# Optimization experiments

Hardware: AMD Instinct MI355X
Metric: run time of the kernel (lower is better)

## Reference

```python
import jax, jax.numpy as jnp
import numpy as np

B, L, D, N = 32, 512, 512, 8  # batch, length, input_size, num_labels


def setup_inputs() -> dict:
    key = jax.random.key(0)
    k1, k2, k3, k4, k5 = jax.random.split(key, 5)
    scale = 0.02
    return {
        "input_h": jax.random.normal(k1, (B, L, D), dtype=jnp.float32),
        "input_c": jax.random.normal(k2, (B, L, D), dtype=jnp.float32),
        "mask": jnp.ones((B, L), dtype=jnp.float32),
        "U": jax.random.normal(k3, (N, D, D), dtype=jnp.float32) * scale,
        "W_d": jax.random.normal(k4, (N, D), dtype=jnp.float32) * scale,
        "W_e": jax.random.normal(k5, (N, D), dtype=jnp.float32) * scale,
        "b": jnp.zeros((N, 1, 1), dtype=jnp.float32),
    }


def reference(input_h, input_c, mask, U, W_d, W_e, b):
    # Biaffine attention (NeuroNLP2 BiAAttention): head = decoder side, child = encoder side.
    # bilinear term: [b, n, l_head, l_child]
    out = jnp.einsum("bld,nde,bme->bnlm", input_h, U, input_c)
    # linear head term -> broadcast over child axis
    out = out + jnp.einsum("nd,bld->bnl", W_d, input_h)[:, :, :, None]
    # linear child term -> broadcast over head axis
    out = out + jnp.einsum("nd,bmd->bnm", W_e, input_c)[:, :, None, :]
    out = out + b[None]  # bias [n,1,1]
    # mask_d / mask_e multiplicative masking
    out = out * mask[:, None, :, None] * mask[:, None, None, :]
    # -inf on the diagonal (no self-arcs)
    length = out.shape[-1]
    diag = jnp.where(jnp.eye(length, dtype=bool), -jnp.inf, 0.0).astype(out.dtype)
    return out + diag
```

## Files before the change

kernel.cpp:

```cpp
#include <hip/hip_runtime.h>


#define B_ 32
#define L_ 512
#define D_ 512
#define N_ 8
#define MT 64
#define STR 536

using f16x8 = __attribute__((ext_vector_type(8))) _Float16;
using f32x4 = __attribute__((ext_vector_type(4))) float;
using u16x8 = __attribute__((ext_vector_type(8))) unsigned short;

static __device__ __forceinline__ float bf2f(unsigned short h) {
  union { unsigned u; float f; } v; v.u = (unsigned)h << 16; return v.f;
}
static __device__ __forceinline__ float h2f(unsigned short h) {
  _Float16 x; __builtin_memcpy(&x, &h, 2); return (float)x;
}
static __device__ __forceinline__ unsigned short f2h(float f) {
  _Float16 x = (_Float16)f; unsigned short u; __builtin_memcpy(&u, &x, 2); return u;
}

static __device__ __forceinline__ int sniff(const unsigned* mkw) {
  const unsigned w = *mkw;
  if (w == 0x3F800000u) return 0;
  if (w == 0x3C003C00u) return 1;
  if (w == 0x3F803F80u) return 2;
  return 1;
}

static __device__ __forceinline__ float ldscal(const void* base, int idx, int flag) {
  if (flag == 0) return ((const float*)base)[idx];
  const unsigned short u = ((const unsigned short*)base)[idx];
  return (flag == 1) ? h2f(u) : bf2f(u);
}

__global__ __launch_bounds__(256)
void cvt_f16(const void* __restrict__ src, unsigned short* __restrict__ dst, int n8,
             const unsigned* __restrict__ mkw) {
  const int flag = sniff(mkw);
  int i = blockIdx.x * 256 + threadIdx.x;
  const int stride = gridDim.x * 256;
  for (; i < n8; i += stride) {
    u16x8 o;
    if (flag == 1) {
      o = ((const u16x8*)src)[i];
    } else if (flag == 0) {
      const float4* s = (const float4*)src + 2 * (size_t)i;
      float4 a = s[0], b = s[1];
      o[0]=f2h(a.x); o[1]=f2h(a.y); o[2]=f2h(a.z); o[3]=f2h(a.w);
      o[4]=f2h(b.x); o[5]=f2h(b.y); o[6]=f2h(b.z); o[7]=f2h(b.w);
    } else {
      u16x8 v = ((const u16x8*)src)[i];
#pragma unroll
      for (int j = 0; j < 8; ++j) o[j] = f2h(bf2f(v[j]));
    }
    *(u16x8*)(dst + 8 * (size_t)i) = o;
  }
}

template <bool CVT>
__global__ __launch_bounds__(512)
void biaffine(const unsigned short* __restrict__ Hc, const void* __restrict__ Hr,
              const unsigned short* __restrict__ Cc, const void* __restrict__ Cr,
              const unsigned short* __restrict__ Uc, const void* __restrict__ Ur,
              const void* __restrict__ Mk, const void* __restrict__ Wd,
              const void* __restrict__ We, const void* __restrict__ Bia,
              unsigned short* __restrict__ Out)
{
  __shared__ __align__(16) unsigned short cpb[64 * STR];
  __shared__ float wev[512], wdv[512], mlv[512], psum[512];
  __shared__ float colterm[64], mcv[64];

  const int flag = sniff((const unsigned*)Mk);
  const int tid  = threadIdx.x;
  const int wave = tid >> 6;
  const int lane = tid & 63;
  const int quad = lane >> 4;
  const int l16  = lane & 15;

  const int bid = blockIdx.x;
  const int n  = bid & 7;
  const int mt = (bid >> 3) & 7;
  const int b  = bid >> 6;

  const size_t cOff = ((size_t)b * L_ + mt * MT) * D_;
  const size_t hOff = (size_t)b * L_ * D_;
  const size_t uOff = (size_t)n * D_ * D_;

  auto ld8 = [&](const void* base, size_t off) -> u16x8 {
    u16x8 o;
    if (flag == 1) {
      o = *(const u16x8*)((const unsigned short*)base + off);
    } else if (flag == 0) {
      const float4* p = (const float4*)((const float*)base + off);
      float4 a = p[0], bq = p[1];
      o[0]=f2h(a.x); o[1]=f2h(a.y); o[2]=f2h(a.z); o[3]=f2h(a.w);
      o[4]=f2h(bq.x); o[5]=f2h(bq.y); o[6]=f2h(bq.z); o[7]=f2h(bq.w);
    } else {
      u16x8 v = *(const u16x8*)((const unsigned short*)base + off);
#pragma unroll
      for (int j = 0; j < 8; ++j) o[j] = f2h(bf2f(v[j]));
    }
    return o;
  };

  {
    const int row = tid >> 3, cb0 = (tid & 7) * 64;
    u16x8* dst = (u16x8*)&cpb[row * STR + cb0];
#pragma unroll
    for (int j = 0; j < 8; ++j) {
      if constexpr (CVT) dst[j] = ld8(Cr, cOff + (size_t)row * D_ + cb0 + j * 8);
      else               dst[j] = ((const u16x8*)(Cc + cOff + (size_t)row * D_ + cb0))[j];
    }
  }
  wev[tid] = ldscal(We, n * D_ + tid, flag);
  wdv[tid] = ldscal(Wd, n * D_ + tid, flag);
  mlv[tid] = ldscal(Mk, b * L_ + tid, flag);
  if (tid < 64) mcv[tid] = ldscal(Mk, b * L_ + mt * MT + tid, flag);
  __syncthreads();

  {
    const int m = tid >> 3, e0 = (tid & 7) * 64;
    float s = 0.f;
#pragma unroll 8
    for (int e = 0; e < 64; ++e) s += h2f(cpb[m * STR + e0 + e]) * wev[e0 + e];
    psum[tid] = s;
  }
  __syncthreads();
  if (tid < 64) {
    float s = ldscal(Bia, n, flag);
#pragma unroll
    for (int j = 0; j < 8; ++j) s += psum[tid * 8 + j];
    colterm[tid] = s;
  }

  f32x4 acc[4][4];
#pragma unroll
  for (int i = 0; i < 4; ++i)
#pragma unroll
    for (int j = 0; j < 4; ++j) acc[i][j] = (f32x4){0.f, 0.f, 0.f, 0.f};

  {
    size_t uo[4];
#pragma unroll
    for (int di = 0; di < 4; ++di)
      uo[di] = uOff + (size_t)((4 * wave + di) * 16 + l16) * D_ + quad * 8;

    auto ldU = [&](int di, int s) -> f16x8 {
      if constexpr (CVT) { u16x8 t = ld8(Ur, uo[di] + (size_t)s * 32); return *(f16x8*)&t; }
      else               return *(const f16x8*)(Uc + uo[di] + (size_t)s * 32);
    };

    f16x8 bB[2][4];
#pragma unroll
    for (int di = 0; di < 4; ++di) bB[0][di] = ldU(di, 0);

#pragma unroll
    for (int s = 0; s < 16; ++s) {
      const int cur = s & 1;
      if (s < 15) {
#pragma unroll
        for (int di = 0; di < 4; ++di) bB[cur ^ 1][di] = ldU(di, s + 1);
      }
      f16x8 aF[4];
#pragma unroll
      for (int mi = 0; mi < 4; ++mi)
        aF[mi] = *(const f16x8*)&cpb[(mi * 16 + l16) * STR + s * 32 + quad * 8];
#pragma unroll
      for (int mi = 0; mi < 4; ++mi)
#pragma unroll
        for (int di = 0; di < 4; ++di)
          acc[mi][di] = __builtin_amdgcn_mfma_f32_16x16x32_f16(aF[mi], bB[cur][di], acc[mi][di], 0, 0, 0);
    }
  }
  __syncthreads();

#pragma unroll
  for (int di = 0; di < 4; ++di) {
    const int d_g = (4 * wave + di) * 16 + l16;
    const float wd = wdv[d_g];
#pragma unroll
    for (int mi = 0; mi < 4; ++mi)
#pragma unroll
      for (int r = 0; r < 4; ++r) {
        const int m_loc = mi * 16 + quad * 4 + r;
        cpb[m_loc * STR + d_g] = f2h(acc[mi][di][r] + wd);
      }
  }
  __syncthreads();

  f32x4 acc2[4][4];
#pragma unroll
  for (int i = 0; i < 4; ++i)
#pragma unroll
    for (int j = 0; j < 4; ++j) acc2[i][j] = (f32x4){0.f, 0.f, 0.f, 0.f};

  {
    size_t ho[4];
#pragma unroll
    for (int li = 0; li < 4; ++li)
      ho[li] = hOff + (size_t)((4 * wave + li) * 16 + l16) * D_ + quad * 8;

    auto ldH = [&](int li, int s) -> f16x8 {
      if constexpr (CVT) { u16x8 t = ld8(Hr, ho[li] + (size_t)s * 32); return *(f16x8*)&t; }
      else               return *(const f16x8*)(Hc + ho[li] + (size_t)s * 32);
    };

    f16x8 aB[2][4];
#pragma unroll
    for (int li = 0; li < 4; ++li) aB[0][li] = ldH(li, 0);

#pragma unroll
    for (int s = 0; s < 16; ++s) {
      const int cur = s & 1;
      if (s < 15) {
#pragma unroll
        for (int li = 0; li < 4; ++li) aB[cur ^ 1][li] = ldH(li, s + 1);
      }
      f16x8 bF[4];
#pragma unroll
      for (int mj = 0; mj < 4; ++mj)
        bF[mj] = *(const f16x8*)&cpb[(mj * 16 + l16) * STR + s * 32 + quad * 8];
#pragma unroll
      for (int li = 0; li < 4; ++li)
#pragma unroll
        for (int mj = 0; mj < 4; ++mj)
          acc2[li][mj] = __builtin_amdgcn_mfma_f32_16x16x32_f16(aB[cur][li], bF[mj], acc2[li][mj], 0, 0, 0);
    }
  }

  const size_t outBase = (size_t)(b * N_ + n) * L_ * L_;
#pragma unroll
  for (int mj = 0; mj < 4; ++mj) {
    const int m_loc = mj * 16 + l16;
    const int m_g = mt * MT + m_loc;
    const float cm = colterm[m_loc];
    const float mm = mcv[m_loc];
#pragma unroll
    for (int li = 0; li < 4; ++li)
#pragma unroll
      for (int r = 0; r < 4; ++r) {
        const int l = (4 * wave + li) * 16 + quad * 4 + r;
        const float v = (acc2[li][mj][r] + cm) * (mlv[l] * mm);
        const unsigned short us = (l == m_g) ? (unsigned short)0xFBFFu : f2h(v);
        Out[outBase + (size_t)l * L_ + m_g] = us;
      }
  }
}

extern "C" void kernel_launch(void* const* d_in, const int* in_sizes, int n_in,
                              void* d_out, int out_size, void* d_ws, size_t ws_size,
                              hipStream_t stream) {
  const void* Hr  = d_in[0];
  const void* Cr  = d_in[1];
  const void* Mk  = d_in[2];
  const void* Ur  = d_in[3];
  const void* Wd  = d_in[4];
  const void* We  = d_in[5];
  const void* Bia = d_in[6];
  unsigned short* Out = (unsigned short*)d_out;
  (void)in_sizes; (void)n_in; (void)out_size;

  const size_t nH = (size_t)B_ * L_ * D_;
  const size_t nC = nH;
  const size_t nU = (size_t)N_ * D_ * D_;
  const size_t needBytes = (nH + nC + nU) * sizeof(unsigned short);

  dim3 grid(B_ * N_ * (L_ / MT));
  dim3 block(512);

  if (ws_size >= needBytes) {
    unsigned short* Hc = (unsigned short*)d_ws;
    unsigned short* Cc = Hc + nH;
    unsigned short* Uc = Cc + nC;
    const unsigned* mkw = (const unsigned*)Mk;
    cvt_f16<<<1024, 256, 0, stream>>>(Hr, Hc, (int)(nH / 8), mkw);
    cvt_f16<<<1024, 256, 0, stream>>>(Cr, Cc, (int)(nC / 8), mkw);
    cvt_f16<<<512,  256, 0, stream>>>(Ur, Uc, (int)(nU / 8), mkw);
    biaffine<false><<<grid, block, 0, stream>>>(Hc, nullptr, Cc, nullptr, Uc, nullptr,
                                                Mk, Wd, We, Bia, Out);
  } else {
    biaffine<true><<<grid, block, 0, stream>>>(nullptr, Hr, nullptr, Cr, nullptr, Ur,
                                               Mk, Wd, We, Bia, Out);
  }
}
```

Before: 575.6 us.

## Precompute child linear term in C conversion pass and merge conversion kernels

Adds a prep_c kernel that converts input_c to fp16 and computes the W_e·c + bias column term for all labels in one pass. The main biaffine kernel can then load that term instead of recomputing it per block with an extra sync. The H and U conversions are merged into one launch, the first U and H fragment loads are issued earlier, and s_setprio is placed around the MFMA bursts. The cost is an extra workspace buffer and a new code path that only runs when the workspace is large enough.

```diff
diff --git a/kernel.cpp b/kernel.cpp
--- a/kernel.cpp
+++ b/kernel.cpp
@@ -34,6 +34,23 @@
   if (flag == 0) return ((const float*)base)[idx];
   const unsigned short u = ((const unsigned short*)base)[idx];
   return (flag == 1) ? h2f(u) : bf2f(u);
+}
+
+static __device__ __forceinline__ u16x8 ld8f(const void* base, size_t off, int flag) {
+  u16x8 o;
+  if (flag == 1) {
+    o = *(const u16x8*)((const unsigned short*)base + off);
+  } else if (flag == 0) {
+    const float4* p = (const float4*)((const float*)base + off);
+    float4 a = p[0], bq = p[1];
+    o[0]=f2h(a.x); o[1]=f2h(a.y); o[2]=f2h(a.z); o[3]=f2h(a.w);
+    o[4]=f2h(bq.x); o[5]=f2h(bq.y); o[6]=f2h(bq.z); o[7]=f2h(bq.w);
+  } else {
+    u16x8 v = *(const u16x8*)((const unsigned short*)base + off);
+#pragma unroll
+    for (int j = 0; j < 8; ++j) o[j] = f2h(bf2f(v[j]));
+  }
+  return o;
 }
 
 __global__ __launch_bounds__(256)
@@ -43,34 +60,94 @@
   int i = blockIdx.x * 256 + threadIdx.x;
   const int stride = gridDim.x * 256;
   for (; i < n8; i += stride) {
-    u16x8 o;
-    if (flag == 1) {
-      o = ((const u16x8*)src)[i];
-    } else if (flag == 0) {
-      const float4* s = (const float4*)src + 2 * (size_t)i;
-      float4 a = s[0], b = s[1];
-      o[0]=f2h(a.x); o[1]=f2h(a.y); o[2]=f2h(a.z); o[3]=f2h(a.w);
-      o[4]=f2h(b.x); o[5]=f2h(b.y); o[6]=f2h(b.z); o[7]=f2h(b.w);
-    } else {
-      u16x8 v = ((const u16x8*)src)[i];
-#pragma unroll
-      for (int j = 0; j < 8; ++j) o[j] = f2h(bf2f(v[j]));
-    }
+    u16x8 o = ld8f(src, 8 * (size_t)i, flag);
     *(u16x8*)(dst + 8 * (size_t)i) = o;
   }
 }
 
-template <bool CVT>
+__global__ __launch_bounds__(256)
+void cvt_f16_2(const void* __restrict__ s0, unsigned short* __restrict__ d0, int n0,
+               const void* __restrict__ s1, unsigned short* __restrict__ d1, int n1,
+               const unsigned* __restrict__ mkw) {
+  const int flag = sniff(mkw);
+  int i = blockIdx.x * 256 + threadIdx.x;
+  const int stride = gridDim.x * 256;
+  const int tot = n0 + n1;
+  for (; i < tot; i += stride) {
+    const void* src; unsigned short* dst; int k;
+    if (i < n0) { src = s0; dst = d0; k = i; }
+    else        { src = s1; dst = d1; k = i - n0; }
+    u16x8 o = ld8f(src, 8 * (size_t)k, flag);
+    *(u16x8*)(dst + 8 * (size_t)k) = o;
+  }
+}
+
+__global__ __launch_bounds__(256)
+void prep_c(const void* __restrict__ Cr, unsigned short* __restrict__ Cc,
+            float* __restrict__ CTp, const void* __restrict__ We,
+            const void* __restrict__ Bia, const unsigned* __restrict__ mkw)
+{
+  __shared__ float wetab[N_ * 512];
+  __shared__ float psum[256 * 9];
+  const int flag = sniff(mkw);
+  const int tid = threadIdx.x;
+  const int b  = blockIdx.x >> 4;
+  const int mc = blockIdx.x & 15;
+
+  for (int i = tid; i < N_ * 512; i += 256) wetab[i] = ldscal(We, i, flag);
+  __syncthreads();
+
+  const int ml = tid >> 3;
+  const int e8 = tid & 7;
+  const int m  = mc * 32 + ml;
+  const size_t rowOff = ((size_t)b * L_ + m) * D_;
+
+  float pn[N_];
+#pragma unroll
+  for (int nn = 0; nn < N_; ++nn) pn[nn] = 0.f;
+
+#pragma unroll
+  for (int j = 0; j < 8; ++j) {
+    const int e0 = (j * 8 + e8) * 8;
+    u16x8 v = ld8f(Cr, rowOff + e0, flag);
+    *(u16x8*)(Cc + rowOff + e0) = v;
+    float cf[8];
+#pragma unroll
+    for (int k = 0; k < 8; ++k) cf[k] = h2f(v[k]);
+#pragma unroll
+    for (int nn = 0; nn < N_; ++nn) {
+      float s = pn[nn];
+#pragma unroll
+      for (int k = 0; k < 8; ++k) s += cf[k] * wetab[nn * 512 + e0 + k];
+      pn[nn] = s;
+    }
+  }
+#pragma unroll
+  for (int nn = 0; nn < N_; ++nn) psum[tid * 9 + nn] = pn[nn];
+  __syncthreads();
+
+  {
+    const int row = tid >> 3, nn = tid & 7;
+    float s = ldscal(Bia, nn, flag);
+#pragma unroll
+    for (int q = 0; q < 8; ++q) s += psum[(row * 8 + q) * 9 + nn];
+    CTp[((size_t)(b * N_ + nn)) * L_ + mc * 32 + row] = s;
+  }
+}
+
+template <bool CVT, bool CT>
 __global__ __launch_bounds__(512)
 void biaffine(const unsigned short* __restrict__ Hc, const void* __restrict__ Hr,
               const unsigned short* __restrict__ Cc, const void* __restrict__ Cr,
               const unsigned short* __restrict__ Uc, const void* __restrict__ Ur,
+              const float* __restrict__ CTp,
               const void* __restrict__ Mk, const void* __restrict__ Wd,
               const void* __restrict__ We, const void* __restrict__ Bia,
               unsigned short* __restrict__ Out)
 {
   __shared__ __align__(16) unsigned short cpb[64 * STR];
-  __shared__ float wev[512], wdv[512], mlv[512], psum[512];
+  __shared__ float wdv[512], mlv[512];
+  __shared__ float wev[512], psum[512];
   __shared__ float colterm[64], mcv[64];
 
   const int flag = sniff((const unsigned*)Mk);
@@ -89,51 +166,59 @@
   const size_t hOff = (size_t)b * L_ * D_;
   const size_t uOff = (size_t)n * D_ * D_;
 
-  auto ld8 = [&](const void* base, size_t off) -> u16x8 {
-    u16x8 o;
-    if (flag == 1) {
-      o = *(const u16x8*)((const unsigned short*)base + off);
-    } else if (flag == 0) {
-      const float4* p = (const float4*)((const float*)base + off);
-      float4 a = p[0], bq = p[1];
-      o[0]=f2h(a.x); o[1]=f2h(a.y); o[2]=f2h(a.z); o[3]=f2h(a.w);
-      o[4]=f2h(bq.x); o[5]=f2h(bq.y); o[6]=f2h(bq.z); o[7]=f2h(bq.w);
-    } else {
-      u16x8 v = *(const u16x8*)((const unsigned short*)base + off);
-#pragma unroll
-      for (int j = 0; j < 8; ++j) o[j] = f2h(bf2f(v[j]));
-    }
-    return o;
+  auto ld8 = [&](const void* base, size_t off) -> u16x8 { return ld8f(base, off, flag); };
+
+  size_t uo[4];
+#pragma unroll
+  for (int di = 0; di < 4; ++di)
+    uo[di] = uOff + (size_t)((4 * wave + di) * 16 + l16) * D_ + quad * 8;
+
+  auto ldU = [&](int di, int s) -> f16x8 {
+    if constexpr (CVT) { u16x8 t = ld8(Ur, uo[di] + (size_t)s * 32); return *(f16x8*)&t; }
+    else               return *(const f16x8*)(Uc + uo[di] + (size_t)s * 32);
   };
+
+  f16x8 bB[2][4];
+#pragma unroll
+  for (int di = 0; di < 4; ++di) bB[0][di] = ldU(di, 0);
 
   {
     const int row = tid >> 3, cb0 = (tid & 7) * 64;
+    u16x8 t[8];
+#pragma unroll
+    for (int j = 0; j < 8; ++j) {
+      if constexpr (CVT) t[j] = ld8(Cr, cOff + (size_t)row * D_ + cb0 + j * 8);
+      else               t[j] = ((const u16x8*)(Cc + cOff + (size_t)row * D_ + cb0))[j];
+    }
     u16x8* dst = (u16x8*)&cpb[row * STR + cb0];
 #pragma unroll
-    for (int j = 0; j < 8; ++j) {
-      if constexpr (CVT) dst[j] = ld8(Cr, cOff + (size_t)row * D_ + cb0 + j * 8);
-      else               dst[j] = ((const u16x8*)(Cc + cOff + (size_t)row * D_ + cb0))[j];
-    }
-  }
-  wev[tid] = ldscal(We, n * D_ + tid, flag);
+    for (int j = 0; j < 8; ++j) dst[j] = t[j];
+  }
   wdv[tid] = ldscal(Wd, n * D_ + tid, flag);
   mlv[tid] = ldscal(Mk, b * L_ + tid, flag);
   if (tid < 64) mcv[tid] = ldscal(Mk, b * L_ + mt * MT + tid, flag);
-  __syncthreads();
-
-  {
-    const int m = tid >> 3, e0 = (tid & 7) * 64;
-    float s = 0.f;
+  if constexpr (CT) {
+    if (tid < 64) colterm[tid] = CTp[((size_t)(b * N_ + n)) * L_ + mt * MT + tid];
+  } else {
+    wev[tid] = ldscal(We, n * D_ + tid, flag);
+  }
+  __syncthreads();
+
+  if constexpr (!CT) {
+    {
+      const int m = tid >> 3, e0 = (tid & 7) * 64;
+      float s = 0.f;
 #pragma unroll 8
-    for (int e = 0; e < 64; ++e) s += h2f(cpb[m * STR + e0 + e]) * wev[e0 + e];
-    psum[tid] = s;
-  }
-  __syncthreads();
-  if (tid < 64) {
-    float s = ldscal(Bia, n, flag);
-#pragma unroll
-    for (int j = 0; j < 8; ++j) s += psum[tid * 8 + j];
-    colterm[tid] = s;
+      for (int e = 0; e < 64; ++e) s += h2f(cpb[m * STR + e0 + e]) * wev[e0 + e];
+      psum[tid] = s;
+    }
+    __syncthreads();
+    if (tid < 64) {
+      float s = ldscal(Bia, n, flag);
+#pragma unroll
+      for (int j = 0; j < 8; ++j) s += psum[tid * 8 + j];
+      colterm[tid] = s;
+    }
   }
 
   f32x4 acc[4][4];
@@ -142,39 +227,40 @@
 #pragma unroll
     for (int j = 0; j < 4; ++j) acc[i][j] = (f32x4){0.f, 0.f, 0.f, 0.f};
 
-  {
-    size_t uo[4];
-#pragma unroll
-    for (int di = 0; di < 4; ++di)
-      uo[di] = uOff + (size_t)((4 * wave + di) * 16 + l16) * D_ + quad * 8;
-
-    auto ldU = [&](int di, int s) -> f16x8 {
-      if constexpr (CVT) { u16x8 t = ld8(Ur, uo[di] + (size_t)s * 32); return *(f16x8*)&t; }
-      else               return *(const f16x8*)(Uc + uo[di] + (size_t)s * 32);
-    };
-
-    f16x8 bB[2][4];
-#pragma unroll
-    for (int di = 0; di < 4; ++di) bB[0][di] = ldU(di, 0);
-
-#pragma unroll
-    for (int s = 0; s < 16; ++s) {
-      const int cur = s & 1;
-      if (s < 15) {
-#pragma unroll
-        for (int di = 0; di < 4; ++di) bB[cur ^ 1][di] = ldU(di, s + 1);
-      }
-      f16x8 aF[4];
-#pragma unroll
-      for (int mi = 0; mi < 4; ++mi)
-        aF[mi] = *(const f16x8*)&cpb[(mi * 16 + l16) * STR + s * 32 + quad * 8];
-#pragma unroll
-      for (int mi = 0; mi < 4; ++mi)
-#pragma unroll
-        for (int di = 0; di < 4; ++di)
-          acc[mi][di] = __builtin_amdgcn_mfma_f32_16x16x32_f16(aF[mi], bB[cur][di], acc[mi][di], 0, 0, 0);
-    }
-  }
+#pragma unroll
+  for (int s = 0; s < 16; ++s) {
+    const int cur = s & 1;
+    if (s < 15) {
+#pragma unroll
+      for (int di = 0; di < 4; ++di) bB[cur ^ 1][di] = ldU(di, s + 1);
+    }
+    f16x8 aF[4];
+#pragma unroll
+    for (int mi = 0; mi < 4; ++mi)
+      aF[mi] = *(const f16x8*)&cpb[(mi * 16 + l16) * STR + s * 32 + quad * 8];
+    __builtin_amdgcn_s_setprio(1);
+#pragma unroll
+    for (int mi = 0; mi < 4; ++mi)
+#pragma unroll
+      for (int di = 0; di < 4; ++di)
+        acc[mi][di] = __builtin_amdgcn_mfma_f32_16x16x32_f16(aF[mi], bB[cur][di], acc[mi][di], 0, 0, 0);
+    __builtin_amdgcn_s_setprio(0);
+  }
+
+  size_t ho[4];
+#pragma unroll
+  for (int li = 0; li < 4; ++li)
+    ho[li] = hOff + (size_t)((4 * wave + li) * 16 + l16) * D_ + quad * 8;
+
+  auto ldH = [&](int li, int s) -> f16x8 {
+    if constexpr (CVT) { u16x8 t = ld8(Hr, ho[li] + (size_t)s * 32); return *(f16x8*)&t; }
+    else               return *(const f16x8*)(Hc + ho[li] + (size_t)s * 32);
+  };
+
+  f16x8 aB[2][4];
+#pragma unroll
+  for (int li = 0; li < 4; ++li) aB[0][li] = ldH(li, 0);
+
   __syncthreads();
 
 #pragma unroll
@@ -197,38 +283,24 @@
 #pragma unroll
     for (int j = 0; j < 4; ++j) acc2[i][j] = (f32x4){0.f, 0.f, 0.f, 0.f};
 
-  {
-    size_t ho[4];
+#pragma unroll
+  for (int s = 0; s < 16; ++s) {
+    const int cur = s & 1;
+    if (s < 15) {
+#pragma unroll
+      for (int li = 0; li < 4; ++li) aB[cur ^ 1][li] = ldH(li, s + 1);
+    }
+    f16x8 bF[4];
+#pragma unroll
+    for (int mj = 0; mj < 4; ++mj)
+      bF[mj] = *(const f16x8*)&cpb[(mj * 16 + l16) * STR + s * 32 + quad * 8];
+    __builtin_amdgcn_s_setprio(1);
 #pragma unroll
     for (int li = 0; li < 4; ++li)
-      ho[li] = hOff + (size_t)((4 * wave + li) * 16 + l16) * D_ + quad * 8;
-
-    auto ldH = [&](int li, int s) -> f16x8 {
-      if constexpr (CVT) { u16x8 t = ld8(Hr, ho[li] + (size_t)s * 32); return *(f16x8*)&t; }
-      else               return *(const f16x8*)(Hc + ho[li] + (size_t)s * 32);
-    };
-
-    f16x8 aB[2][4];
-#pragma unroll
-    for (int li = 0; li < 4; ++li) aB[0][li] = ldH(li, 0);
-
-#pragma unroll
-    for (int s = 0; s < 16; ++s) {
-      const int cur = s & 1;
-      if (s < 15) {
-#pragma unroll
-        for (int li = 0; li < 4; ++li) aB[cur ^ 1][li] = ldH(li, s + 1);
-      }
-      f16x8 bF[4];
 #pragma unroll
       for (int mj = 0; mj < 4; ++mj)
-        bF[mj] = *(const f16x8*)&cpb[(mj * 16 + l16) * STR + s * 32 + quad * 8];
-#pragma unroll
-      for (int li = 0; li < 4; ++li)
-#pragma unroll
-        for (int mj = 0; mj < 4; ++mj)
-          acc2[li][mj] = __builtin_amdgcn_mfma_f32_16x16x32_f16(aB[cur][li], bF[mj], acc2[li][mj], 0, 0, 0);
-    }
+        acc2[li][mj] = __builtin_amdgcn_mfma_f32_16x16x32_f16(aB[cur][li], bF[mj], acc2[li][mj], 0, 0, 0);
+    __builtin_amdgcn_s_setprio(0);
   }
 
   const size_t outBase = (size_t)(b * N_ + n) * L_ * L_;
@@ -266,23 +338,34 @@
   const size_t nH = (size_t)B_ * L_ * D_;
   const size_t nC = nH;
   const size_t nU = (size_t)N_ * D_ * D_;
-  const size_t needBytes = (nH + nC + nU) * sizeof(unsigned short);
+  const size_t ctN = (size_t)B_ * N_ * L_;
+  const size_t needHalf = (nH + nC + nU) * sizeof(unsigned short);
+  const size_t needFull = needHalf + ctN * sizeof(float);
 
   dim3 grid(B_ * N_ * (L_ / MT));
   dim3 block(512);
-
-  if (ws_size >= needBytes) {
+  const unsigned* mkw = (const unsigned*)Mk;
+
+  if (ws_size >= needFull) {
     unsigned short* Hc = (unsigned short*)d_ws;
     unsigned short* Cc = Hc + nH;
     unsigned short* Uc = Cc + nC;
-    const unsigned* mkw = (const unsigned*)Mk;
+    float* CTp = (float*)(Uc + nU);
+    prep_c<<<512, 256, 0, stream>>>(Cr, Cc, CTp, We, Bia, mkw);
+    cvt_f16_2<<<2048, 256, 0, stream>>>(Hr, Hc, (int)(nH / 8), Ur, Uc, (int)(nU / 8), mkw);
+    biaffine<false, true><<<grid, block, 0, stream>>>(Hc, nullptr, Cc, nullptr, Uc, nullptr,
+                                                      CTp, Mk, Wd, We, Bia, Out);
+  } else if (ws_size >= needHalf) {
+    unsigned short* Hc = (unsigned short*)d_ws;
+    unsigned short* Cc = Hc + nH;
+    unsigned short* Uc = Cc + nC;
     cvt_f16<<<1024, 256, 0, stream>>>(Hr, Hc, (int)(nH / 8), mkw);
     cvt_f16<<<1024, 256, 0, stream>>>(Cr, Cc, (int)(nC / 8), mkw);
     cvt_f16<<<512,  256, 0, stream>>>(Ur, Uc, (int)(nU / 8), mkw);
-    biaffine<false><<<grid, block, 0, stream>>>(Hc, nullptr, Cc, nullptr, Uc, nullptr,
-                                                Mk, Wd, We, Bia, Out);
+    biaffine<false, false><<<grid, block, 0, stream>>>(Hc, nullptr, Cc, nullptr, Uc, nullptr,
+                                                       nullptr, Mk, Wd, We, Bia, Out);
   } else {
-    biaffine<true><<<grid, block, 0, stream>>>(nullptr, Hr, nullptr, Cr, nullptr, Ur,
-                                               Mk, Wd, We, Bia, Out);
-  }
-}
+    biaffine<true, false><<<grid, block, 0, stream>>>(nullptr, Hr, nullptr, Cr, nullptr, Ur,
+                                                      nullptr, Mk, Wd, We, Bia, Out);
+  }
+}
```

Result: slower. 588.2 us (+2.2%).
